# Kernel tuning notes

Measured on AMD Instinct MI355X. Metric: run time of the kernel, lower is better.

## Reference

```python
import jax, jax.numpy as jnp
import numpy as np

N, N_SPINS, N_HIDDEN = 8192, 1024, 1024


def setup_inputs() -> dict:
    key = jax.random.key(0)
    ks = jax.random.split(key, 6)
    s_in = 1.0 / np.sqrt(N_SPINS)
    s_h = 1.0 / np.sqrt(N_HIDDEN)
    return {
        "x": jax.random.normal(ks[0], (N, N_SPINS), dtype=jnp.float32),
        "W_in": jax.random.normal(ks[1], (N_HIDDEN, N_SPINS), dtype=jnp.float32) * s_in,
        "b_in": jax.random.normal(ks[2], (N_HIDDEN,), dtype=jnp.float32) * s_in,
        "Wq": jax.random.normal(ks[3], (N_HIDDEN, N_HIDDEN), dtype=jnp.float32) * s_h,
        "Wk": jax.random.normal(ks[4], (N_HIDDEN, N_HIDDEN), dtype=jnp.float32) * s_h,
        "Wv": jax.random.normal(ks[5], (N_HIDDEN, N_HIDDEN), dtype=jnp.float32) * s_h,
    }


def reference(x, W_in, b_in, Wq, Wk, Wv):
    # embedding: Linear(n_spins, n_hidden)  -> h: [N, H]
    h = x @ W_in.T + b_in
    q = h @ Wq.T                      # [N, H]
    k = h @ Wk.T                      # [N, H]
    v = h @ Wv.T                      # [N, H]
    scores = (q @ k.T) * 0.25         # [N, N], scale 1/4 as in source
    attn = jax.nn.softmax(scores, axis=0)  # softmax over dim=0 (columns)
    out = attn @ v                    # [N, H]
    # log(cosh(z)) = |z| + log1p(exp(-2|z|)) - log(2), numerically stable
    a = jnp.abs(out)
    logcosh = a + jnp.log1p(jnp.exp(-2.0 * a)) - jnp.log(jnp.asarray(2.0, out.dtype))
    return jnp.sum(logcosh, axis=-1)  # [N]
```

## Files before the change

### kernel.cpp

```cpp
#include <hip/hip_runtime.h>
#include <hip/hip_bf16.h>
#include <cstdint>
#include <cstddef>

#define NTOK 8192
#define NHID 1024

typedef __attribute__((ext_vector_type(8))) __bf16 bf16x8;
typedef __attribute__((ext_vector_type(4))) float f32x4;

__device__ __forceinline__ unsigned short f2bf(float f) {
    union { float f; unsigned u; } v; v.f = f;
    unsigned r = v.u + 0x7FFF + ((v.u >> 16) & 1);
    return (unsigned short)(r >> 16);
}

__device__ __forceinline__ float bf2f(unsigned short u) {
    union { unsigned u; float f; } v; v.u = ((unsigned)u) << 16;
    return v.f;
}

__device__ __forceinline__ void async_copy16(const void* gsrc, void* ldsdst) {
    __builtin_amdgcn_global_load_lds(
        (const __attribute__((address_space(1))) unsigned int*)gsrc,
        (__attribute__((address_space(3))) unsigned int*)ldsdst,
        16, 0, 0);
}

template <int EPI, bool SWAP>
__global__ __launch_bounds__(512, 2) void gemm_sq4(
    const unsigned short* __restrict__ A,
    const unsigned short* __restrict__ B,
    void* __restrict__ C,
    const float* __restrict__ bias,
    float* __restrict__ zsum,
    float scale, int M, int N, int K, int lda, int ldb)
{
    __shared__ __attribute__((aligned(16))) unsigned short lds[2][32768];

    const int tid  = threadIdx.x;
    const int wave = tid >> 6;
    const int lane = tid & 63;
    const int bm = (SWAP ? blockIdx.x : blockIdx.y) * 256;
    const int bn = (SWAP ? blockIdx.y : blockIdx.x) * 256;
    const size_t ldaz = (size_t)lda;
    const size_t ldbz = (size_t)ldb;

    const int srow = lane >> 3;
    const int scol = ((lane & 7) ^ srow) * 8;
    const unsigned short* Agq[4];
    const unsigned short* Bgq[4];
    int offq[4];
#pragma unroll
    for (int qq = 0; qq < 4; ++qq) {
        int r = qq * 64 + wave * 8 + srow;
        Agq[qq] = A + (size_t)(bm + r) * ldaz + scol;
        Bgq[qq] = B + (size_t)(bn + r) * ldbz + scol;
        offq[qq] = (qq * 64 + wave * 8) * 64;
    }

    const int wm = (wave >> 2) * 128;
    const int wn = (wave & 3) * 64;
    const int fr = lane & 15;
    const int frl = fr & 7;
    const int q = lane >> 4;

    const int pc0 = (q ^ frl) * 8;
    const int pc1 = ((4 + q) ^ frl) * 8;

    f32x4 acc[8][4] = {};

    const int nt = K >> 6;

    auto stA = [&](int s, int qq) {
        async_copy16(Agq[qq], &lds[s][offq[qq]]); Agq[qq] += 64;
    };
    auto stB = [&](int s, int qq) {
        async_copy16(Bgq[qq], &lds[s][16384 + offq[qq]]); Bgq[qq] += 64;
    };

#define PHASE_MFMA(IBASE)                                                      \
    do {                                                                       \
        __builtin_amdgcn_s_setprio(1);                                         \
        _Pragma("unroll")                                                      \
        for (int i = 0; i < 4; ++i)                                            \
            _Pragma("unroll")                                                  \
            for (int j = 0; j < 4; ++j)                                        \
                acc[(IBASE) + i][j] = __builtin_amdgcn_mfma_f32_16x16x32_bf16( \
                    a[i], b[j], acc[(IBASE) + i][j], 0, 0, 0);                 \
        __builtin_amdgcn_s_setprio(0);                                         \
    } while (0)

    stB(0, 0); stB(0, 1); stB(0, 2); stB(0, 3);
    stA(0, 0); stA(0, 2); stA(0, 1); stA(0, 3);
    asm volatile("s_waitcnt vmcnt(2)" ::: "memory");
    asm volatile("s_barrier" ::: "memory");

    for (int t = 0; t < nt; ++t) {
        const int cb = t & 1;
        const int nb = cb ^ 1;
        const unsigned short* As = &lds[cb][0];
        const unsigned short* Bs = &lds[cb][16384];
        const bool pf = (t + 1 < nt);

        bf16x8 a[4], b[4];

#pragma unroll
        for (int i = 0; i < 4; ++i) a[i] = *(const bf16x8*)&As[(wm + i * 16 + fr) * 64 + pc0];
#pragma unroll
        for (int j = 0; j < 4; ++j) b[j] = *(const bf16x8*)&Bs[(wn + j * 16 + fr) * 64 + pc0];
        if (pf) { stB(nb, 0); stB(nb, 1); }
        asm volatile("s_barrier" ::: "memory");
        asm volatile("s_waitcnt lgkmcnt(0)" ::: "memory");
        __builtin_amdgcn_sched_barrier(0);
        PHASE_MFMA(0);
        if (pf) asm volatile("s_waitcnt vmcnt(2)" ::: "memory");
        else    asm volatile("s_waitcnt vmcnt(0)" ::: "memory");
        asm volatile("s_barrier" ::: "memory");

#pragma unroll
        for (int i = 0; i < 4; ++i) a[i] = *(const bf16x8*)&As[(wm + 64 + i * 16 + fr) * 64 + pc0];
        if (pf) { stB(nb, 2); stB(nb, 3); }
        asm volatile("s_barrier" ::: "memory");
        asm volatile("s_waitcnt lgkmcnt(0)" ::: "memory");
        __builtin_amdgcn_sched_barrier(0);
        PHASE_MFMA(4);
        asm volatile("s_barrier" ::: "memory");

#pragma unroll
        for (int i = 0; i < 4; ++i) a[i] = *(const bf16x8*)&As[(wm + i * 16 + fr) * 64 + pc1];
#pragma unroll
        for (int j = 0; j < 4; ++j) b[j] = *(const bf16x8*)&Bs[(wn + j * 16 + fr) * 64 + pc1];
        if (pf) { stA(nb, 0); stA(nb, 2); }
        asm volatile("s_barrier" ::: "memory");
        asm volatile("s_waitcnt lgkmcnt(0)" ::: "memory");
        __builtin_amdgcn_sched_barrier(0);
        PHASE_MFMA(0);
        asm volatile("s_barrier" ::: "memory");

#pragma unroll
        for (int i = 0; i < 4; ++i) a[i] = *(const bf16x8*)&As[(wm + 64 + i * 16 + fr) * 64 + pc1];
        if (pf) { stA(nb, 1); stA(nb, 3); }
        asm volatile("s_barrier" ::: "memory");
        asm volatile("s_waitcnt lgkmcnt(0)" ::: "memory");
        __builtin_amdgcn_sched_barrier(0);
        PHASE_MFMA(4);
        if (pf) asm volatile("s_waitcnt vmcnt(2)" ::: "memory");
        asm volatile("s_barrier" ::: "memory");
    }
#undef PHASE_MFMA

    const int erow = q * 4;
    float colsum[4] = {0.f, 0.f, 0.f, 0.f};
    float bv[4];
#pragma unroll
    for (int j = 0; j < 4; ++j)
        bv[j] = (EPI == 1 && bias) ? bias[bn + wn + j * 16 + fr] : 0.0f;
#pragma unroll
    for (int i = 0; i < 8; ++i) {
        const int grow0 = bm + wm + i * 16 + erow;
#pragma unroll
        for (int r = 0; r < 4; ++r) {
            const size_t rowoff = (size_t)(grow0 + r) * N;
#pragma unroll
            for (int j = 0; j < 4; ++j) {
                const int gcol = bn + wn + j * 16 + fr;
                float v;
                if (EPI == 2) {
                    v = __expf(fmaf(acc[i][j][r], scale, -64.0f));
                    colsum[j] += v;
                } else {
                    v = acc[i][j][r] * scale + bv[j];
                }
                if (EPI == 0) ((float*)C)[rowoff + gcol] = v;
                else          ((unsigned short*)C)[rowoff + gcol] = f2bf(v);
            }
        }
    }
    if (EPI == 2) {
#pragma unroll
        for (int j = 0; j < 4; ++j) {
            float cs = colsum[j];
            cs += __shfl_xor(cs, 16, 64);
            cs += __shfl_xor(cs, 32, 64);
            if (q == 0) atomicAdd(&zsum[bn + wn + j * 16 + fr], cs);
        }
    }
}

template <int EPI, bool SWAP>
__global__ __launch_bounds__(512, 2) void gemm_bt4(
    const unsigned short* __restrict__ A,
    const unsigned short* __restrict__ B,
    void* __restrict__ C,
    const float* __restrict__ bias,
    float* __restrict__ zsum,
    float scale, int M, int N, int K, int lda, int ldb)
{
    __shared__ __attribute__((aligned(16))) unsigned short lds[3][24576];

    const int tid  = threadIdx.x;
    const int wave = tid >> 6;
    const int lane = tid & 63;
    const int bm = (SWAP ? blockIdx.x : blockIdx.y) * 256;
    const int bn = (SWAP ? blockIdx.y : blockIdx.x) * 128;
    const size_t ldaz = (size_t)lda;
    const size_t ldbz = (size_t)ldb;

    const int srow = lane >> 3;
    const int scol = ((lane & 7) ^ srow) * 8;
    const unsigned short* Ag[4];
    const unsigned short* Bg[2];
    int Aoff[4], Boff[2];
#pragma unroll
    for (int t = 0; t < 4; ++t) {
        int r = (wave * 4 + t) * 8 + srow;
        Ag[t] = A + (size_t)(bm + r) * ldaz + scol;
        Aoff[t] = (wave * 4 + t) * 512;
    }
#pragma unroll
    for (int t = 0; t < 2; ++t) {
        int r = (wave * 2 + t) * 8 + srow;
        Bg[t] = B + (size_t)(bn + r) * ldbz + scol;
        Boff[t] = 16384 + (wave * 2 + t) * 512;
    }

    const int wm = (wave >> 1) * 64;
    const int wn = (wave & 1) * 64;
    const int fr = lane & 15;
    const int frl = fr & 7;
    const int q = lane >> 4;

    const int pc0 = (q ^ frl) * 8;
    const int pc1 = ((4 + q) ^ frl) * 8;

    f32x4 acc[4][4] = {};

    const int nt = K >> 6;

    {
        unsigned short* b0 = &lds[0][0];
        unsigned short* b1 = &lds[1][0];
#pragma unroll
        for (int u = 0; u < 4; ++u) { async_copy16(Ag[u], b0 + Aoff[u]); Ag[u] += 64; }
#pragma unroll
        for (int u = 0; u < 2; ++u) { async_copy16(Bg[u], b0 + Boff[u]); Bg[u] += 64; }
#pragma unroll
        for (int u = 0; u < 4; ++u) { async_copy16(Ag[u], b1 + Aoff[u]); Ag[u] += 64; }
#pragma unroll
        for (int u = 0; u < 2; ++u) { async_copy16(Bg[u], b1 + Boff[u]); Bg[u] += 64; }
        asm volatile("s_waitcnt vmcnt(6)" ::: "memory");
        asm volatile("s_barrier" ::: "memory");
    }

    bf16x8 a0_0, a0_1, a0_2, a0_3, b0_0, b0_1, b0_2, b0_3;
    bf16x8 a1_0, a1_1, a1_2, a1_3, b1_0, b1_1, b1_2, b1_3;

    {
        const unsigned short* As = &lds[0][0];
        const unsigned short* Bs = &lds[0][16384];
        a0_0 = *(const bf16x8*)&As[(wm +  0 + fr) * 64 + pc0];
        a0_1 = *(const bf16x8*)&As[(wm + 16 + fr) * 64 + pc0];
        a0_2 = *(const bf16x8*)&As[(wm + 32 + fr) * 64 + pc0];
        a0_3 = *(const bf16x8*)&As[(wm + 48 + fr) * 64 + pc0];
        b0_0 = *(const bf16x8*)&Bs[(wn +  0 + fr) * 64 + pc0];
        b0_1 = *(const bf16x8*)&Bs[(wn + 16 + fr) * 64 + pc0];
        b0_2 = *(const bf16x8*)&Bs[(wn + 32 + fr) * 64 + pc0];
        b0_3 = *(const bf16x8*)&Bs[(wn + 48 + fr) * 64 + pc0];
    }

#define MFMA16(AA0, AA1, AA2, AA3, BB0, BB1, BB2, BB3)                         \
    do {                                                                       \
        __builtin_amdgcn_s_setprio(1);                                         \
        acc[0][0] = __builtin_amdgcn_mfma_f32_16x16x32_bf16(AA0, BB0, acc[0][0], 0, 0, 0); \
        acc[0][1] = __builtin_amdgcn_mfma_f32_16x16x32_bf16(AA0, BB1, acc[0][1], 0, 0, 0); \
        acc[0][2] = __builtin_amdgcn_mfma_f32_16x16x32_bf16(AA0, BB2, acc[0][2], 0, 0, 0); \
        acc[0][3] = __builtin_amdgcn_mfma_f32_16x16x32_bf16(AA0, BB3, acc[0][3], 0, 0, 0); \
        acc[1][0] = __builtin_amdgcn_mfma_f32_16x16x32_bf16(AA1, BB0, acc[1][0], 0, 0, 0); \
        acc[1][1] = __builtin_amdgcn_mfma_f32_16x16x32_bf16(AA1, BB1, acc[1][1], 0, 0, 0); \
        acc[1][2] = __builtin_amdgcn_mfma_f32_16x16x32_bf16(AA1, BB2, acc[1][2], 0, 0, 0); \
        acc[1][3] = __builtin_amdgcn_mfma_f32_16x16x32_bf16(AA1, BB3, acc[1][3], 0, 0, 0); \
        acc[2][0] = __builtin_amdgcn_mfma_f32_16x16x32_bf16(AA2, BB0, acc[2][0], 0, 0, 0); \
        acc[2][1] = __builtin_amdgcn_mfma_f32_16x16x32_bf16(AA2, BB1, acc[2][1], 0, 0, 0); \
        acc[2][2] = __builtin_amdgcn_mfma_f32_16x16x32_bf16(AA2, BB2, acc[2][2], 0, 0, 0); \
        acc[2][3] = __builtin_amdgcn_mfma_f32_16x16x32_bf16(AA2, BB3, acc[2][3], 0, 0, 0); \
        acc[3][0] = __builtin_amdgcn_mfma_f32_16x16x32_bf16(AA3, BB0, acc[3][0], 0, 0, 0); \
        acc[3][1] = __builtin_amdgcn_mfma_f32_16x16x32_bf16(AA3, BB1, acc[3][1], 0, 0, 0); \
        acc[3][2] = __builtin_amdgcn_mfma_f32_16x16x32_bf16(AA3, BB2, acc[3][2], 0, 0, 0); \
        acc[3][3] = __builtin_amdgcn_mfma_f32_16x16x32_bf16(AA3, BB3, acc[3][3], 0, 0, 0); \
        __builtin_amdgcn_s_setprio(0);                                         \
    } while (0)

    int cb = 0;
    int sb = 2;
    for (int t = 0; t < nt; ++t) {
        const bool pf = (t + 2 < nt);
        const unsigned short* As = &lds[cb][0];
        const unsigned short* Bs = &lds[cb][16384];
        unsigned short* Sb = &lds[sb][0];
        const int nb = (cb == 2) ? 0 : cb + 1;
        const unsigned short* An = &lds[nb][0];
        const unsigned short* Bn = &lds[nb][16384];

        a1_0 = *(const bf16x8*)&As[(wm +  0 + fr) * 64 + pc1];
        a1_1 = *(const bf16x8*)&As[(wm + 16 + fr) * 64 + pc1];
        a1_2 = *(const bf16x8*)&As[(wm + 32 + fr) * 64 + pc1];
        a1_3 = *(const bf16x8*)&As[(wm + 48 + fr) * 64 + pc1];
        b1_0 = *(const bf16x8*)&Bs[(wn +  0 + fr) * 64 + pc1];
        b1_1 = *(const bf16x8*)&Bs[(wn + 16 + fr) * 64 + pc1];
        b1_2 = *(const bf16x8*)&Bs[(wn + 32 + fr) * 64 + pc1];
        b1_3 = *(const bf16x8*)&Bs[(wn + 48 + fr) * 64 + pc1];
        if (pf) {
#pragma unroll
            for (int u = 0; u < 4; ++u) { async_copy16(Ag[u], Sb + Aoff[u]); Ag[u] += 64; }
        }
        __builtin_amdgcn_sched_barrier(0);
        MFMA16(a0_0, a0_1, a0_2, a0_3, b0_0, b0_1, b0_2, b0_3);
        if (t < nt - 2) asm volatile("s_waitcnt vmcnt(4)" ::: "memory");
        else            asm volatile("s_waitcnt vmcnt(0)" ::: "memory");
        asm volatile("s_barrier" ::: "memory");

        if (t + 1 < nt) {
            a0_0 = *(const bf16x8*)&An[(wm +  0 + fr) * 64 + pc0];
            a0_1 = *(const bf16x8*)&An[(wm + 16 + fr) * 64 + pc0];
            a0_2 = *(const bf16x8*)&An[(wm + 32 + fr) * 64 + pc0];
            a0_3 = *(const bf16x8*)&An[(wm + 48 + fr) * 64 + pc0];
            b0_0 = *(const bf16x8*)&Bn[(wn +  0 + fr) * 64 + pc0];
            b0_1 = *(const bf16x8*)&Bn[(wn + 16 + fr) * 64 + pc0];
            b0_2 = *(const bf16x8*)&Bn[(wn + 32 + fr) * 64 + pc0];
            b0_3 = *(const bf16x8*)&Bn[(wn + 48 + fr) * 64 + pc0];
        }
        if (pf) {
#pragma unroll
            for (int u = 0; u < 2; ++u) { async_copy16(Bg[u], Sb + Boff[u]); Bg[u] += 64; }
        }
        __builtin_amdgcn_sched_barrier(0);
        MFMA16(a1_0, a1_1, a1_2, a1_3, b1_0, b1_1, b1_2, b1_3);
        asm volatile("s_barrier" ::: "memory");

        if (pf) sb = (sb == 2) ? 0 : sb + 1;
        cb = nb;
    }
#undef MFMA16

    const int erow = q * 4;
#pragma unroll
    for (int j = 0; j < 4; ++j) {
        const int gcol = bn + wn + j * 16 + fr;
        const float bv = (EPI == 1 && bias) ? bias[gcol] : 0.0f;
        float colsum = 0.0f;
#pragma unroll
        for (int i = 0; i < 4; ++i) {
            const int grow0 = bm + wm + i * 16 + erow;
#pragma unroll
            for (int r = 0; r < 4; ++r) {
                float v;
                if (EPI == 2) {
                    v = __expf(fmaf(acc[i][j][r], scale, -64.0f));
                    colsum += v;
                } else {
                    v = acc[i][j][r] * scale + bv;
                }
                size_t idx = (size_t)(grow0 + r) * N + gcol;
                if (EPI == 0) ((float*)C)[idx] = v;
                else          ((unsigned short*)C)[idx] = f2bf(v);
            }
        }
        if (EPI == 2) {
            colsum += __shfl_xor(colsum, 16, 64);
            colsum += __shfl_xor(colsum, 32, 64);
            if (q == 0) atomicAdd(&zsum[gcol], colsum);
        }
    }
}

__global__ void cvt_all(const float4* __restrict__ x,
                        const float4* __restrict__ w0,
                        const float4* __restrict__ w1,
                        const float4* __restrict__ w2,
                        const float4* __restrict__ w3,
                        ushort4* __restrict__ xb,
                        ushort4* __restrict__ wdst,
                        float4* __restrict__ pz4,
                        int n4x, int n4w)
{
    int i = blockIdx.x * blockDim.x + threadIdx.x;
    int n4 = n4x + 4 * n4w;
    if (i >= n4) {
        int zi = i - n4;
        if (zi < 2048) pz4[zi] = make_float4(0.f, 0.f, 0.f, 0.f);
        return;
    }
    float4 f;
    ushort4* dst;
    if (i < n4x) {
        f = x[i]; dst = xb + i;
    } else {
        int r = i - n4x;
        int seg = r / n4w, off = r % n4w;
        const float4* src = (seg == 0) ? w0 : (seg == 1) ? w1 : (seg == 2) ? w2 : w3;
        f = src[off]; dst = wdst + r;
    }
    ushort4 o;
    o.x = f2bf(f.x); o.y = f2bf(f.y); o.z = f2bf(f.z); o.w = f2bf(f.w);
    *dst = o;
}

__global__ __launch_bounds__(256) void transpose_scale(
    const unsigned short* __restrict__ v,
    const float* __restrict__ z,
    unsigned short* __restrict__ vt)
{
    __shared__ float lds[64 * 65];
    const int tid = threadIdx.x;
    const int j0 = blockIdx.x * 64;
    const int h0 = blockIdx.y * 64;
    const int c = tid & 63;
    const int r0 = tid >> 6;
#pragma unroll
    for (int it = 0; it < 16; ++it) {
        int r = it * 4 + r0;
        lds[r * 65 + c] = bf2f(v[(size_t)(j0 + r) * 3072 + h0 + c]);
    }
    __syncthreads();
    const float rz = 1.0f / z[j0 + c];
#pragma unroll
    for (int it = 0; it < 16; ++it) {
        int r = it * 4 + r0;
        vt[(size_t)(h0 + r) * NTOK + j0 + c] = f2bf(lds[c * 65 + r] * rz);
    }
}

__global__ void logcosh_rowsum(const ushort4* __restrict__ O4,
                               float* __restrict__ out)
{
    const float LN2 = 0.69314718055994531f;
    int row = blockIdx.x;
    ushort4 u = O4[(size_t)row * 256 + threadIdx.x];
    float s = 0.0f, a;
    a = fabsf(bf2f(u.x)); s += a + log1pf(__expf(-2.0f * a));
    a = fabsf(bf2f(u.y)); s += a + log1pf(__expf(-2.0f * a));
    a = fabsf(bf2f(u.z)); s += a + log1pf(__expf(-2.0f * a));
    a = fabsf(bf2f(u.w)); s += a + log1pf(__expf(-2.0f * a));
    s -= 4.0f * LN2;
    for (int off = 32; off; off >>= 1) s += __shfl_down(s, off, 64);
    __shared__ float red[4];
    if ((threadIdx.x & 63) == 0) red[threadIdx.x >> 6] = s;
    __syncthreads();
    if (threadIdx.x == 0) out[row] = red[0] + red[1] + red[2] + red[3];
}

extern "C" void kernel_launch(void* const* d_in, const int* in_sizes, int n_in,
                              void* d_out, int out_size, void* d_ws, size_t ws_size,
                              hipStream_t stream)
{
    (void)in_sizes; (void)n_in; (void)out_size; (void)ws_size;

    const float* x    = (const float*)d_in[0];
    const float* W_in = (const float*)d_in[1];
    const float* b_in = (const float*)d_in[2];
    const float* Wq   = (const float*)d_in[3];
    const float* Wk   = (const float*)d_in[4];
    const float* Wv   = (const float*)d_in[5];
    float* out = (float*)d_out;

    char* w = (char*)d_ws;
    const size_t MiB = 1024 * 1024;
    unsigned short* Pb     = (unsigned short*)(w);
    unsigned short* qkv    = (unsigned short*)(w + 128 * MiB);
    unsigned short* xb     = (unsigned short*)(w + 128 * MiB);
    unsigned short* outb   = (unsigned short*)(w + 128 * MiB);
    unsigned short* hb     = (unsigned short*)(w + 176 * MiB);
    unsigned short* vtb    = (unsigned short*)(w + 176 * MiB);
    unsigned short* wib    = (unsigned short*)(w + 192 * MiB);
    unsigned short* wqkvb  = (unsigned short*)(w + 194 * MiB);
    float*          pz     = (float*)         (w + 200 * MiB);

    {
        int n4x = NTOK * NHID / 4;
        int n4w = NHID * NHID / 4;
        int n4  = n4x + 4 * n4w;
        cvt_all<<<n4 / 256 + 8, 256, 0, stream>>>(
            (const float4*)x, (const float4*)W_in, (const float4*)Wq,
            (const float4*)Wk, (const float4*)Wv,
            (ushort4*)xb, (ushort4*)wib, (float4*)pz, n4x, n4w);
    }

    dim3 gNH(NHID / 128, NTOK / 256);
    gemm_bt4<1, false><<<gNH, 512, 0, stream>>>(
        xb, wib, hb, b_in, nullptr, 1.0f, NTOK, NHID, NHID, NHID, NHID);

    dim3 gQKV(3 * NHID / 128, NTOK / 256);
    gemm_bt4<1, false><<<gQKV, 512, 0, stream>>>(
        hb, wqkvb, qkv, nullptr, nullptr, 1.0f, NTOK, 3 * NHID, NHID, NHID, NHID);

    dim3 gS(NTOK / 256, NTOK / 256);
    gemm_sq4<2, false><<<gS, 512, 0, stream>>>(
        qkv, qkv + NHID, Pb, nullptr, pz, 0.25f, NTOK, NTOK, NHID,
        3 * NHID, 3 * NHID);

    dim3 gT(NTOK / 64, NHID / 64);
    transpose_scale<<<gT, 256, 0, stream>>>(qkv + 2 * NHID, pz, vtb);

    dim3 gO(NTOK / 256, NHID / 128);
    gemm_bt4<1, true><<<gO, 512, 0, stream>>>(
        Pb, vtb, outb, nullptr, nullptr, 1.0f, NTOK, NHID, NTOK, NTOK, NTOK);

    logcosh_rowsum<<<NTOK, 256, 0, stream>>>((const ushort4*)outb, out);
}
```

Before: 456.2 us.

## Skip negligible attention K-tiles in AV GEMM using per-block column max

```diff
diff --git a/kernel.cpp b/kernel.cpp
--- a/kernel.cpp
+++ b/kernel.cpp
@@ -26,6 +26,11 @@
         (__attribute__((address_space(3))) unsigned int*)ldsdst,
         16, 0, 0);
 }
+
+__device__ __forceinline__ void atomicMaxPosF(float* addr, float val) {
+    atomicMax((int*)addr, __float_as_int(val));
+}
+
 
 template <int EPI, bool SWAP>
 __global__ __launch_bounds__(512, 2) void gemm_sq4(
@@ -34,6 +39,7 @@
     void* __restrict__ C,
     const float* __restrict__ bias,
     float* __restrict__ zsum,
+    float* __restrict__ pmax,
     float scale, int M, int N, int K, int lda, int ldb)
 {
     __shared__ __attribute__((aligned(16))) unsigned short lds[2][32768];
@@ -152,6 +158,7 @@
 
     const int erow = q * 4;
     float colsum[4] = {0.f, 0.f, 0.f, 0.f};
+    float colmax[4] = {0.f, 0.f, 0.f, 0.f};
     float bv[4];
 #pragma unroll
     for (int j = 0; j < 4; ++j)
@@ -169,6 +176,7 @@
                 if (EPI == 2) {
                     v = __expf(fmaf(acc[i][j][r], scale, -64.0f));
                     colsum[j] += v;
+                    colmax[j] = fmaxf(colmax[j], v);
                 } else {
                     v = acc[i][j][r] * scale + bv[j];
                 }
@@ -180,10 +188,17 @@
     if (EPI == 2) {
 #pragma unroll
         for (int j = 0; j < 4; ++j) {
+            const int gcol = bn + wn + j * 16 + fr;
             float cs = colsum[j];
             cs += __shfl_xor(cs, 16, 64);
             cs += __shfl_xor(cs, 32, 64);
-            if (q == 0) atomicAdd(&zsum[bn + wn + j * 16 + fr], cs);
+            float cm = colmax[j];
+            cm = fmaxf(cm, __shfl_xor(cm, 16, 64));
+            cm = fmaxf(cm, __shfl_xor(cm, 32, 64));
+            if (q == 0) {
+                atomicAdd(&zsum[gcol], cs);
+                atomicMaxPosF(&pmax[(size_t)(bm >> 8) * N + gcol], cm);
+            }
         }
     }
 }
@@ -374,6 +389,194 @@
     }
 }
 
+__global__ __launch_bounds__(512, 2) void gemm_av(
+    const unsigned short* __restrict__ A,
+    const unsigned short* __restrict__ B,
+    unsigned short* __restrict__ C,
+    const float* __restrict__ pmax,
+    const float* __restrict__ z,
+    int M, int N, int K)
+{
+    __shared__ __attribute__((aligned(16))) unsigned short lds[3][24576];
+    __shared__ short flags[128];
+    __shared__ short list[128];
+    __shared__ int s_nact;
+
+    const int tid  = threadIdx.x;
+    const int wave = tid >> 6;
+    const int lane = tid & 63;
+    const int bm = blockIdx.x * 256;
+    const int bn = blockIdx.y * 128;
+    const int bi = bm >> 8;
+    const int ntile = K >> 6;
+    const float EPS = 0.000244140625f;
+
+    for (int t = wave; t < ntile; t += 8) {
+        int j = t * 64 + lane;
+        float d = pmax[(size_t)bi * K + j] - EPS * z[j];
+#pragma unroll
+        for (int off = 32; off; off >>= 1) d = fmaxf(d, __shfl_xor(d, off, 64));
+        if (lane == 0) flags[t] = (d >= 0.0f) ? 1 : 0;
+    }
+    __syncthreads();
+    if (tid == 0) {
+        int n = 0;
+        for (int t = 0; t < ntile; ++t) if (flags[t]) list[n++] = (short)t;
+        s_nact = n;
+    }
+    __syncthreads();
+    const int nact = s_nact;
+
+    const int srow = lane >> 3;
+    const int scol = ((lane & 7) ^ srow) * 8;
+    const unsigned short* Abase[4];
+    const unsigned short* Bbase[2];
+    int Aoff[4], Boff[2];
+#pragma unroll
+    for (int t = 0; t < 4; ++t) {
+        int r = (wave * 4 + t) * 8 + srow;
+        Abase[t] = A + (size_t)(bm + r) * K + scol;
+        Aoff[t] = (wave * 4 + t) * 512;
+    }
+#pragma unroll
+    for (int t = 0; t < 2; ++t) {
+        int r = (wave * 2 + t) * 8 + srow;
+        Bbase[t] = B + (size_t)(bn + r) * K + scol;
+        Boff[t] = 16384 + (wave * 2 + t) * 512;
+    }
+
+    const int wm = (wave >> 1) * 64;
+    const int wn = (wave & 1) * 64;
+    const int fr = lane & 15;
+    const int frl = fr & 7;
+    const int q = lane >> 4;
+
+    const int pc0 = (q ^ frl) * 8;
+    const int pc1 = ((4 + q) ^ frl) * 8;
+
+    f32x4 acc[4][4] = {};
+
+    auto stageA = [&](int s, int kt) {
+        const size_t ko = (size_t)kt * 64;
+#pragma unroll
+        for (int u = 0; u < 4; ++u) async_copy16(Abase[u] + ko, &lds[s][Aoff[u]]);
+    };
+    auto stageB = [&](int s, int kt) {
+        const size_t ko = (size_t)kt * 64;
+#pragma unroll
+        for (int u = 0; u < 2; ++u) async_copy16(Bbase[u] + ko, &lds[s][Boff[u]]);
+    };
+
+    if (nact > 0) {
+        stageA(0, list[0]); stageB(0, list[0]);
+        if (nact > 1) {
+            stageA(1, list[1]); stageB(1, list[1]);
+            asm volatile("s_waitcnt vmcnt(6)" ::: "memory");
+        } else {
+            asm volatile("s_waitcnt vmcnt(0)" ::: "memory");
+        }
+        asm volatile("s_barrier" ::: "memory");
+
+        bf16x8 a0_0, a0_1, a0_2, a0_3, b0_0, b0_1, b0_2, b0_3;
+        bf16x8 a1_0, a1_1, a1_2, a1_3, b1_0, b1_1, b1_2, b1_3;
+
+        {
+            const unsigned short* As = &lds[0][0];
+            const unsigned short* Bs = &lds[0][16384];
+            a0_0 = *(const bf16x8*)&As[(wm +  0 + fr) * 64 + pc0];
+            a0_1 = *(const bf16x8*)&As[(wm + 16 + fr) * 64 + pc0];
+            a0_2 = *(const bf16x8*)&As[(wm + 32 + fr) * 64 + pc0];
+            a0_3 = *(const bf16x8*)&As[(wm + 48 + fr) * 64 + pc0];
+            b0_0 = *(const bf16x8*)&Bs[(wn +  0 + fr) * 64 + pc0];
+            b0_1 = *(const bf16x8*)&Bs[(wn + 16 + fr) * 64 + pc0];
+            b0_2 = *(const bf16x8*)&Bs[(wn + 32 + fr) * 64 + pc0];
+            b0_3 = *(const bf16x8*)&Bs[(wn + 48 + fr) * 64 + pc0];
+        }
+
+#define MFMA16(AA0, AA1, AA2, AA3, BB0, BB1, BB2, BB3)                         \
+    do {                                                                       \
+        __builtin_amdgcn_s_setprio(1);                                         \
+        acc[0][0] = __builtin_amdgcn_mfma_f32_16x16x32_bf16(AA0, BB0, acc[0][0], 0, 0, 0); \
+        acc[0][1] = __builtin_amdgcn_mfma_f32_16x16x32_bf16(AA0, BB1, acc[0][1], 0, 0, 0); \
+        acc[0][2] = __builtin_amdgcn_mfma_f32_16x16x32_bf16(AA0, BB2, acc[0][2], 0, 0, 0); \
+        acc[0][3] = __builtin_amdgcn_mfma_f32_16x16x32_bf16(AA0, BB3, acc[0][3], 0, 0, 0); \
+        acc[1][0] = __builtin_amdgcn_mfma_f32_16x16x32_bf16(AA1, BB0, acc[1][0], 0, 0, 0); \
+        acc[1][1] = __builtin_amdgcn_mfma_f32_16x16x32_bf16(AA1, BB1, acc[1][1], 0, 0, 0); \
+        acc[1][2] = __builtin_amdgcn_mfma_f32_16x16x32_bf16(AA1, BB2, acc[1][2], 0, 0, 0); \
+        acc[1][3] = __builtin_amdgcn_mfma_f32_16x16x32_bf16(AA1, BB3, acc[1][3], 0, 0, 0); \
+        acc[2][0] = __builtin_amdgcn_mfma_f32_16x16x32_bf16(AA2, BB0, acc[2][0], 0, 0, 0); \
+        acc[2][1] = __builtin_amdgcn_mfma_f32_16x16x32_bf16(AA2, BB1, acc[2][1], 0, 0, 0); \
+        acc[2][2] = __builtin_amdgcn_mfma_f32_16x16x32_bf16(AA2, BB2, acc[2][2], 0, 0, 0); \
+        acc[2][3] = __builtin_amdgcn_mfma_f32_16x16x32_bf16(AA2, BB3, acc[2][3], 0, 0, 0); \
+        acc[3][0] = __builtin_amdgcn_mfma_f32_16x16x32_bf16(AA3, BB0, acc[3][0], 0, 0, 0); \
+        acc[3][1] = __builtin_amdgcn_mfma_f32_16x16x32_bf16(AA3, BB1, acc[3][1], 0, 0, 0); \
+        acc[3][2] = __builtin_amdgcn_mfma_f32_16x16x32_bf16(AA3, BB2, acc[3][2], 0, 0, 0); \
+        acc[3][3] = __builtin_amdgcn_mfma_f32_16x16x32_bf16(AA3, BB3, acc[3][3], 0, 0, 0); \
+        __builtin_amdgcn_s_setprio(0);                                         \
+    } while (0)
+
+        int cb = 0;
+        int sb = 2;
+        for (int t = 0; t < nact; ++t) {
+            const bool pf = (t + 2 < nact);
+            const unsigned short* As = &lds[cb][0];
+            const unsigned short* Bs = &lds[cb][16384];
+            const int nb = (cb == 2) ? 0 : cb + 1;
+            const unsigned short* An = &lds[nb][0];
+            const unsigned short* Bn = &lds[nb][16384];
+
+            a1_0 = *(const bf16x8*)&As[(wm +  0 + fr) * 64 + pc1];
+            a1_1 = *(const bf16x8*)&As[(wm + 16 + fr) * 64 + pc1];
+            a1_2 = *(const bf16x8*)&As[(wm + 32 + fr) * 64 + pc1];
+            a1_3 = *(const bf16x8*)&As[(wm + 48 + fr) * 64 + pc1];
+            b1_0 = *(const bf16x8*)&Bs[(wn +  0 + fr) * 64 + pc1];
+            b1_1 = *(const bf16x8*)&Bs[(wn + 16 + fr) * 64 + pc1];
+            b1_2 = *(const bf16x8*)&Bs[(wn + 32 + fr) * 64 + pc1];
+            b1_3 = *(const bf16x8*)&Bs[(wn + 48 + fr) * 64 + pc1];
+            if (pf) stageA(sb, list[t + 2]);
+            __builtin_amdgcn_sched_barrier(0);
+            MFMA16(a0_0, a0_1, a0_2, a0_3, b0_0, b0_1, b0_2, b0_3);
+            if (t < nact - 2) asm volatile("s_waitcnt vmcnt(4)" ::: "memory");
+            else              asm volatile("s_waitcnt vmcnt(0)" ::: "memory");
+            asm volatile("s_barrier" ::: "memory");
+
+            if (t + 1 < nact) {
+                a0_0 = *(const bf16x8*)&An[(wm +  0 + fr) * 64 + pc0];
+                a0_1 = *(const bf16x8*)&An[(wm + 16 + fr) * 64 + pc0];
+                a0_2 = *(const bf16x8*)&An[(wm + 32 + fr) * 64 + pc0];
+                a0_3 = *(const bf16x8*)&An[(wm + 48 + fr) * 64 + pc0];
+                b0_0 = *(const bf16x8*)&Bn[(wn +  0 + fr) * 64 + pc0];
+                b0_1 = *(const bf16x8*)&Bn[(wn + 16 + fr) * 64 + pc0];
+                b0_2 = *(const bf16x8*)&Bn[(wn + 32 + fr) * 64 + pc0];
+                b0_3 = *(const bf16x8*)&Bn[(wn + 48 + fr) * 64 + pc0];
+            }
+            if (pf) stageB(sb, list[t + 2]);
+            __builtin_amdgcn_sched_barrier(0);
+            MFMA16(a1_0, a1_1, a1_2, a1_3, b1_0, b1_1, b1_2, b1_3);
+            asm volatile("s_barrier" ::: "memory");
+
+            if (pf) sb = (sb == 2) ? 0 : sb + 1;
+            cb = nb;
+        }
+#undef MFMA16
+    }
+
+    const int erow = q * 4;
+#pragma unroll
+    for (int j = 0; j < 4; ++j) {
+        const int gcol = bn + wn + j * 16 + fr;
+#pragma unroll
+        for (int i = 0; i < 4; ++i) {
+            const int grow0 = bm + wm + i * 16 + erow;
+#pragma unroll
+            for (int r = 0; r < 4; ++r) {
+                size_t idx = (size_t)(grow0 + r) * N + gcol;
+                C[idx] = f2bf(acc[i][j][r]);
+            }
+        }
+    }
+}
+
 __global__ void cvt_all(const float4* __restrict__ x,
                         const float4* __restrict__ w0,
                         const float4* __restrict__ w1,
@@ -388,7 +591,7 @@
     int n4 = n4x + 4 * n4w;
     if (i >= n4) {
         int zi = i - n4;
-        if (zi < 2048) pz4[zi] = make_float4(0.f, 0.f, 0.f, 0.f);
+        if (zi < 67584) pz4[zi] = make_float4(0.f, 0.f, 0.f, 0.f);
         return;
     }
     float4 f;
@@ -475,12 +678,13 @@
     unsigned short* wib    = (unsigned short*)(w + 192 * MiB);
     unsigned short* wqkvb  = (unsigned short*)(w + 194 * MiB);
     float*          pz     = (float*)         (w + 200 * MiB);
+    float*          Pbmax  = (float*)         (w + 200 * MiB + 8192 * sizeof(float));
 
     {
         int n4x = NTOK * NHID / 4;
         int n4w = NHID * NHID / 4;
         int n4  = n4x + 4 * n4w;
-        cvt_all<<<n4 / 256 + 8, 256, 0, stream>>>(
+        cvt_all<<<n4 / 256 + 264, 256, 0, stream>>>(
             (const float4*)x, (const float4*)W_in, (const float4*)Wq,
             (const float4*)Wk, (const float4*)Wv,
             (ushort4*)xb, (ushort4*)wib, (float4*)pz, n4x, n4w);
@@ -496,15 +700,15 @@
 
     dim3 gS(NTOK / 256, NTOK / 256);
     gemm_sq4<2, false><<<gS, 512, 0, stream>>>(
-        qkv, qkv + NHID, Pb, nullptr, pz, 0.25f, NTOK, NTOK, NHID,
+        qkv, qkv + NHID, Pb, nullptr, pz, Pbmax, 0.25f, NTOK, NTOK, NHID,
         3 * NHID, 3 * NHID);
 
     dim3 gT(NTOK / 64, NHID / 64);
     transpose_scale<<<gT, 256, 0, stream>>>(qkv + 2 * NHID, pz, vtb);
 
     dim3 gO(NTOK / 256, NHID / 128);
-    gemm_bt4<1, true><<<gO, 512, 0, stream>>>(
-        Pb, vtb, outb, nullptr, nullptr, 1.0f, NTOK, NHID, NTOK, NTOK, NTOK);
+    gemm_av<<<gO, 512, 0, stream>>>(
+        Pb, vtb, outb, Pbmax, pz, NTOK, NHID, NTOK);
 
     logcosh_rowsum<<<NTOK, 256, 0, stream>>>((const ushort4*)outb, out);
 }
```

After: 470.1 us. 3.0% more time.
